# Kernel tuning notes

Measured on AMD Instinct MI355X. Metric: run time of the kernel, lower is better.

The kernel has to match this reference:

```python
import jax, jax.numpy as jnp
import numpy as np

N_NODES = 100000    # nodes in river network
N_PATHS = 1000000   # number of (src, dst) routing paths
MAX_DELAY = 16
DT = 1.0
CASCADE = 1.0
T = int(MAX_DELAY / DT)        # expanded time window (assert in original)
E = 8000000                    # total flattened path-node entries


def setup_inputs() -> dict:
    key = jax.random.key(0)
    k1, k2, k3 = jax.random.split(key, 3)
    params = jax.random.uniform(k1, (N_NODES,), dtype=jnp.float32)
    path_idxs = jnp.sort(jax.random.randint(k2, (E,), 0, N_PATHS, dtype=jnp.int32))
    path_nodes = jax.random.randint(k3, (E,), 0, N_NODES, dtype=jnp.int32)
    return {"params": params, "path_idxs": path_idxs, "path_nodes": path_nodes}


def reference(params, path_idxs, path_nodes):
    # irf_fn 'linear_storage': per-node linear-reservoir impulse response h(t)=exp(-t/k)/k
    k = params + 0.5                                  # storage const in [0.5, 1.5)
    t = jnp.arange(T, dtype=params.dtype) * DT        # [T]
    irfs = jnp.exp(-t[None, :] / k[:, None]) / k[:, None]   # [N, T]
    # frequency domain
    irfs_freq = jnp.fft.rfft(irfs, n=T, axis=-1)      # [N, F] complex
    # irf_agg 'log_triton': cascade-combine IRFs along each path = product of
    # transfer functions, done in log domain: gather logs, segment-sum per path.
    log_freq = jnp.log(irfs_freq)                     # [N, F] complex log
    gathered = log_freq[path_nodes]                   # [E, F] irregular gather
    agg_re = jax.ops.segment_sum(gathered.real, path_idxs, num_segments=N_PATHS)
    agg_im = jax.ops.segment_sum(gathered.imag, path_idxs, num_segments=N_PATHS)
    agg_log = (agg_re + 1j * agg_im) * CASCADE        # [P, F]
    irfs_freq_agg = jnp.exp(agg_log)
    # back to time domain
    irfs_agg = jnp.fft.irfft(irfs_freq_agg, n=T, axis=-1)   # [P, T]
    irfs_agg = jax.nn.relu(irfs_agg)
    irfs_agg = jnp.flip(irfs_agg, -1)                 # sampler.phi_k is identity for dt=1
    irfs_agg = irfs_agg / jnp.sum(irfs_agg, -1, keepdims=True)
    return irfs_agg                                   # COO values; coords scatter is a storage step
```

## Files before the change

### kernel.cpp

```cpp
#include <hip/hip_runtime.h>
#include <math.h>

#define N_NODES  100000
#define N_PATHS  1000000
#define E_TOT    8000000
#define NF       9
#define TAB_U32  25000
#define EB       1024
#define EPT      2
#define PB       256
#define RCH      4096

#define RMIN 0.135330f
#define RMAX 0.513420f
#define QSCALE (255.0f / (RMAX - RMIN))
#define DEQ    ((RMAX - RMIN) / 255.0f)

__device__ __constant__ float COS16[16] = {
  1.0f,  0.92387953f,  0.70710678f,  0.38268343f,  0.0f, -0.38268343f, -0.70710678f, -0.92387953f,
 -1.0f, -0.92387953f, -0.70710678f, -0.38268343f,  0.0f,  0.38268343f,  0.70710678f,  0.92387953f };
__device__ __constant__ float SIN16[16] = {
  0.0f,  0.38268343f,  0.70710678f,  0.92387953f,  1.0f,  0.92387953f,  0.70710678f,  0.38268343f,
  0.0f, -0.38268343f, -0.70710678f, -0.92387953f, -1.0f, -0.92387953f, -0.70710678f, -0.38268343f };

__global__ void node_rq_kernel(const float* __restrict__ params,
                               unsigned char* __restrict__ rtab_q) {
    int n = blockIdx.x * blockDim.x + threadIdx.x;
    if (n >= N_NODES) return;
    float k = params[n] + 0.5f;
    float r = expf(-1.0f / k);
    float q = (r - RMIN) * QSCALE;
    q = fminf(fmaxf(q + 0.5f, 0.0f), 255.0f);
    rtab_q[n] = (unsigned char)q;
}

__device__ __forceinline__ void put_bounds(int a, int b, int e, int* __restrict__ start) {
    for (int p = a + 1; p <= b; ++p) start[p] = e;
}

__global__ __launch_bounds__(EB) void epass_kernel(const int* __restrict__ pidx,
                                                   const int* __restrict__ pnode,
                                                   const unsigned int* __restrict__ rtab_q,
                                                   int* __restrict__ start,
                                                   unsigned char* __restrict__ r8_all) {
    __shared__ unsigned int tab[TAB_U32];
    const unsigned char* tabb = (const unsigned char*)tab;
    int tid = threadIdx.x;
    for (int i = tid; i < TAB_U32; i += EB) tab[i] = rtab_q[i];
    __syncthreads();

    int base_q = blockIdx.x * EB * EPT;
#pragma unroll
    for (int g = 0; g < EPT; g++) {
        int q = base_q + g * EB + tid;
        if (q >= E_TOT / 4) break;
        int e = q * 4;
        int4 v = ((const int4*)pidx)[q];
        int4 w = ((const int4*)pnode)[q];
        uchar4 r;
        r.x = tabb[w.x];
        r.y = tabb[w.y];
        r.z = tabb[w.z];
        r.w = tabb[w.w];
        ((uchar4*)r8_all)[q] = r;
        int prev = (e == 0) ? -1 : pidx[e - 1];
        put_bounds(prev, v.x, e,     start);
        put_bounds(v.x,  v.y, e + 1, start);
        put_bounds(v.y,  v.z, e + 2, start);
        put_bounds(v.z,  v.w, e + 3, start);
        if (e + 4 == E_TOT) {
            for (int p = v.w + 1; p <= N_PATHS; ++p) start[p] = E_TOT;
        }
    }
}

__global__ __launch_bounds__(PB) void path_kernel(const int* __restrict__ start,
                                                  const unsigned char* __restrict__ r8_all,
                                                  float* __restrict__ out) {
    __shared__ unsigned char rch[RCH + 4];
    int tid = threadIdx.x;
    int p0 = blockIdx.x * PB;
    int p  = p0 + tid;
    int pend = (p0 + PB < N_PATHS) ? p0 + PB : N_PATHS;

    int blk_s = start[p0];
    int blk_e = start[pend];
    int s0 = 0, s1 = 0;
    if (p < N_PATHS) { s0 = start[p]; s1 = start[p + 1]; }

    float d0 = 1.0f, d8 = 1.0f;
    float dr[7], di[7];
#pragma unroll
    for (int f = 0; f < 7; f++) { dr[f] = 1.0f; di[f] = 0.0f; }

    const unsigned int* r8w = (const unsigned int*)r8_all;
    for (int ab = blk_s & ~3; ab < blk_e; ab += RCH) {
        int wlen = (blk_e - ab < RCH) ? (blk_e - ab) : RCH;
        int nw = (wlen + 3) >> 2;
        __syncthreads();
        for (int j = tid; j < nw; j += PB)
            ((unsigned int*)rch)[j] = r8w[(ab >> 2) + j];
        __syncthreads();

        int lo = (s0 > ab) ? s0 : ab;
        int hi = (s1 < ab + wlen) ? s1 : ab + wlen;
        int n = hi - lo;
        int bi = lo - ab;
        for (int j = 0; j < n; j += 4) {
            float ra = fmaf((float)rch[bi + j], DEQ, RMIN);
            float rb = (j + 1 < n) ? fmaf((float)rch[bi + j + 1], DEQ, RMIN) : 0.0f;
            float rc = (j + 2 < n) ? fmaf((float)rch[bi + j + 2], DEQ, RMIN) : 0.0f;
            float rd = (j + 3 < n) ? fmaf((float)rch[bi + j + 3], DEQ, RMIN) : 0.0f;
            float sab = ra + rb, qab = ra * rb;
            float scd = rc + rd, qcd = rc * rd;
            float e1 = sab + scd;
            float e2 = fmaf(sab, scd, qab + qcd);
            float e3 = fmaf(qab, scd, qcd * sab);
            float e4 = qab * qcd;
#pragma unroll
            for (int f = 1; f <= 7; f++) {
                float tr = fmaf(-e1, COS16[f], 1.0f);
                tr = fmaf( e2, COS16[(2 * f) & 15], tr);
                tr = fmaf(-e3, COS16[(3 * f) & 15], tr);
                tr = fmaf( e4, COS16[(4 * f) & 15], tr);
                float ti = e1 * SIN16[f];
                ti = fmaf(-e2, SIN16[(2 * f) & 15], ti);
                ti = fmaf( e3, SIN16[(3 * f) & 15], ti);
                ti = fmaf(-e4, SIN16[(4 * f) & 15], ti);
                float a = dr[f - 1], b = di[f - 1];
                dr[f - 1] = fmaf(a, tr, -b * ti);
                di[f - 1] = fmaf(a, ti,  b * tr);
            }
            d0 *= ((1.0f - e1) + (e2 - e3)) + e4;
            d8 *= ((1.0f + e1) + (e2 + e3)) + e4;
        }
    }

    if (p >= N_PATHS) return;

    float Xr[NF], Xi[NF];
    Xr[0] = 1.0f; Xi[0] = 0.0f;
#pragma unroll
    for (int f = 1; f < 8; f++) {
        float a = dr[f - 1], b = di[f - 1];
        float m = fmaf(a, a, b * b);
        float inv = d0 * __builtin_amdgcn_rcpf(m);
        Xr[f] =  a * inv;
        Xi[f] = -b * inv;
    }
    Xr[8] = d0 * __builtin_amdgcn_rcpf(d8); Xi[8] = 0.0f;

    float xt[16];
    float ssum = 0.0f;
#pragma unroll
    for (int t = 0; t < 16; t++) {
        float acc = Xr[0] + ((t & 1) ? -Xr[8] : Xr[8]);
#pragma unroll
        for (int f = 1; f < 8; f++) {
            int kk = (f * t) & 15;
            acc = fmaf(2.0f * Xr[f], COS16[kk], acc);
            acc = fmaf(-2.0f * Xi[f], SIN16[kk], acc);
        }
        acc *= (1.0f / 16.0f);
        acc = fmaxf(acc, 0.0f);
        xt[t] = acc;
        ssum += acc;
    }

    float invs = __builtin_amdgcn_rcpf(ssum);
    float4* op4 = (float4*)(out + (size_t)p * 16);
    op4[0] = make_float4(xt[15] * invs, xt[14] * invs, xt[13] * invs, xt[12] * invs);
    op4[1] = make_float4(xt[11] * invs, xt[10] * invs, xt[9]  * invs, xt[8]  * invs);
    op4[2] = make_float4(xt[7]  * invs, xt[6]  * invs, xt[5]  * invs, xt[4]  * invs);
    op4[3] = make_float4(xt[3]  * invs, xt[2]  * invs, xt[1]  * invs, xt[0]  * invs);
}

extern "C" void kernel_launch(void* const* d_in, const int* in_sizes, int n_in,
                              void* d_out, int out_size, void* d_ws, size_t ws_size,
                              hipStream_t stream) {
    const float* params = (const float*)d_in[0];
    const int* path_idxs = (const int*)d_in[1];
    const int* path_nodes = (const int*)d_in[2];
    float* out = (float*)d_out;

    size_t off_rq    = 0;
    size_t off_start = (off_rq + (size_t)N_NODES + 1023) & ~(size_t)1023;
    size_t off_r8    = (off_start + (size_t)(N_PATHS + 1) * 4 + 1023) & ~(size_t)1023;

    unsigned char* rtab_q = (unsigned char*)d_ws + off_rq;
    int* start = (int*)((char*)d_ws + off_start);
    unsigned char* r8_all = (unsigned char*)d_ws + off_r8;

    {
        int threads = 256;
        int blocks = (N_NODES + threads - 1) / threads;
        node_rq_kernel<<<blocks, threads, 0, stream>>>(params, rtab_q);
    }
    {
        int per_block = EB * EPT;
        int blocks = (E_TOT / 4 + per_block - 1) / per_block;
        epass_kernel<<<blocks, EB, 0, stream>>>(path_idxs, path_nodes,
                                                (const unsigned int*)rtab_q,
                                                start, r8_all);
    }
    {
        int blocks = (N_PATHS + PB - 1) / PB;
        path_kernel<<<blocks, PB, 0, stream>>>(start, r8_all, out);
    }
}
```

Measured before the change: 143.3 us.

## Read path bytes directly from global memory and exploit inverse-DFT symmetry

```diff
diff --git a/kernel.cpp b/kernel.cpp
--- a/kernel.cpp
+++ b/kernel.cpp
@@ -7,9 +7,8 @@
 #define NF       9
 #define TAB_U32  25000
 #define EB       1024
-#define EPT      2
+#define EPT      4
 #define PB       256
-#define RCH      4096
 
 #define RMIN 0.135330f
 #define RMAX 0.513420f
@@ -75,70 +74,59 @@
 }
 
 __global__ __launch_bounds__(PB) void path_kernel(const int* __restrict__ start,
-                                                  const unsigned char* __restrict__ r8_all,
+                                                  const unsigned int* __restrict__ r8w,
                                                   float* __restrict__ out) {
-    __shared__ unsigned char rch[RCH + 4];
-    int tid = threadIdx.x;
-    int p0 = blockIdx.x * PB;
-    int p  = p0 + tid;
-    int pend = (p0 + PB < N_PATHS) ? p0 + PB : N_PATHS;
-
-    int blk_s = start[p0];
-    int blk_e = start[pend];
-    int s0 = 0, s1 = 0;
-    if (p < N_PATHS) { s0 = start[p]; s1 = start[p + 1]; }
+    int p = blockIdx.x * PB + threadIdx.x;
+    if (p >= N_PATHS) return;
+
+    int s0 = start[p];
+    int s1 = start[p + 1];
+    int len = s1 - s0;
+    int nq = (len + 3) >> 2;
+    int a0 = s0 >> 2;
+    unsigned sh = (unsigned)(s0 & 3) * 8u;
 
     float d0 = 1.0f, d8 = 1.0f;
     float dr[7], di[7];
 #pragma unroll
     for (int f = 0; f < 7; f++) { dr[f] = 1.0f; di[f] = 0.0f; }
 
-    const unsigned int* r8w = (const unsigned int*)r8_all;
-    for (int ab = blk_s & ~3; ab < blk_e; ab += RCH) {
-        int wlen = (blk_e - ab < RCH) ? (blk_e - ab) : RCH;
-        int nw = (wlen + 3) >> 2;
-        __syncthreads();
-        for (int j = tid; j < nw; j += PB)
-            ((unsigned int*)rch)[j] = r8w[(ab >> 2) + j];
-        __syncthreads();
-
-        int lo = (s0 > ab) ? s0 : ab;
-        int hi = (s1 < ab + wlen) ? s1 : ab + wlen;
-        int n = hi - lo;
-        int bi = lo - ab;
-        for (int j = 0; j < n; j += 4) {
-            float ra = fmaf((float)rch[bi + j], DEQ, RMIN);
-            float rb = (j + 1 < n) ? fmaf((float)rch[bi + j + 1], DEQ, RMIN) : 0.0f;
-            float rc = (j + 2 < n) ? fmaf((float)rch[bi + j + 2], DEQ, RMIN) : 0.0f;
-            float rd = (j + 3 < n) ? fmaf((float)rch[bi + j + 3], DEQ, RMIN) : 0.0f;
-            float sab = ra + rb, qab = ra * rb;
-            float scd = rc + rd, qcd = rc * rd;
-            float e1 = sab + scd;
-            float e2 = fmaf(sab, scd, qab + qcd);
-            float e3 = fmaf(qab, scd, qcd * sab);
-            float e4 = qab * qcd;
-#pragma unroll
-            for (int f = 1; f <= 7; f++) {
-                float tr = fmaf(-e1, COS16[f], 1.0f);
-                tr = fmaf( e2, COS16[(2 * f) & 15], tr);
-                tr = fmaf(-e3, COS16[(3 * f) & 15], tr);
-                tr = fmaf( e4, COS16[(4 * f) & 15], tr);
-                float ti = e1 * SIN16[f];
-                ti = fmaf(-e2, SIN16[(2 * f) & 15], ti);
-                ti = fmaf( e3, SIN16[(3 * f) & 15], ti);
-                ti = fmaf(-e4, SIN16[(4 * f) & 15], ti);
-                float a = dr[f - 1], b = di[f - 1];
-                dr[f - 1] = fmaf(a, tr, -b * ti);
-                di[f - 1] = fmaf(a, ti,  b * tr);
-            }
-            d0 *= ((1.0f - e1) + (e2 - e3)) + e4;
-            d8 *= ((1.0f + e1) + (e2 + e3)) + e4;
+    unsigned cur = (nq > 0) ? r8w[a0] : 0u;
+    for (int q = 0; q < nq; q++) {
+        int w = a0 + q + 1;
+        unsigned nxt = (w < E_TOT / 4) ? r8w[w] : 0u;
+        unsigned grp = (unsigned)(((((unsigned long long)nxt) << 32) | cur) >> sh);
+        cur = nxt;
+        int rem = len - 4 * q;
+        float ra = fmaf((float)(grp & 255u), DEQ, RMIN);
+        float rb = (rem > 1) ? fmaf((float)((grp >> 8) & 255u), DEQ, RMIN) : 0.0f;
+        float rc = (rem > 2) ? fmaf((float)((grp >> 16) & 255u), DEQ, RMIN) : 0.0f;
+        float rd = (rem > 3) ? fmaf((float)(grp >> 24), DEQ, RMIN) : 0.0f;
+        float sab = ra + rb, qab = ra * rb;
+        float scd = rc + rd, qcd = rc * rd;
+        float e1 = sab + scd;
+        float e2 = fmaf(sab, scd, qab + qcd);
+        float e3 = fmaf(qab, scd, qcd * sab);
+        float e4 = qab * qcd;
+#pragma unroll
+        for (int f = 1; f <= 7; f++) {
+            float tr = fmaf(-e1, COS16[f], 1.0f);
+            tr = fmaf( e2, COS16[(2 * f) & 15], tr);
+            tr = fmaf(-e3, COS16[(3 * f) & 15], tr);
+            tr = fmaf( e4, COS16[(4 * f) & 15], tr);
+            float ti = e1 * SIN16[f];
+            ti = fmaf(-e2, SIN16[(2 * f) & 15], ti);
+            ti = fmaf( e3, SIN16[(3 * f) & 15], ti);
+            ti = fmaf(-e4, SIN16[(4 * f) & 15], ti);
+            float a = dr[f - 1], b = di[f - 1];
+            dr[f - 1] = fmaf(a, tr, -b * ti);
+            di[f - 1] = fmaf(a, ti,  b * tr);
         }
-    }
-
-    if (p >= N_PATHS) return;
-
-    float Xr[NF], Xi[NF];
+        d0 *= ((1.0f - e1) + (e2 - e3)) + e4;
+        d8 *= ((1.0f + e1) + (e2 + e3)) + e4;
+    }
+
+    float Xr[8], Xi[8];
     Xr[0] = 1.0f; Xi[0] = 0.0f;
 #pragma unroll
     for (int f = 1; f < 8; f++) {
@@ -148,23 +136,33 @@
         Xr[f] =  a * inv;
         Xi[f] = -b * inv;
     }
-    Xr[8] = d0 * __builtin_amdgcn_rcpf(d8); Xi[8] = 0.0f;
+    float X8 = d0 * __builtin_amdgcn_rcpf(d8);
 
     float xt[16];
-    float ssum = 0.0f;
-#pragma unroll
-    for (int t = 0; t < 16; t++) {
-        float acc = Xr[0] + ((t & 1) ? -Xr[8] : Xr[8]);
+    float c0 = 0.0f, c8 = 0.0f;
+#pragma unroll
+    for (int f = 1; f < 8; f++) {
+        c0 += 2.0f * Xr[f];
+        c8 += (f & 1) ? -2.0f * Xr[f] : 2.0f * Xr[f];
+    }
+    xt[0] = fmaxf((Xr[0] + X8 + c0) * (1.0f / 16.0f), 0.0f);
+    xt[8] = fmaxf((Xr[0] + X8 + c8) * (1.0f / 16.0f), 0.0f);
+    float ssum = xt[0] + xt[8];
+#pragma unroll
+    for (int t = 1; t < 8; t++) {
+        float Ct = 0.0f, St = 0.0f;
 #pragma unroll
         for (int f = 1; f < 8; f++) {
             int kk = (f * t) & 15;
-            acc = fmaf(2.0f * Xr[f], COS16[kk], acc);
-            acc = fmaf(-2.0f * Xi[f], SIN16[kk], acc);
+            Ct = fmaf(2.0f * Xr[f], COS16[kk], Ct);
+            St = fmaf(2.0f * Xi[f], SIN16[kk], St);
         }
-        acc *= (1.0f / 16.0f);
-        acc = fmaxf(acc, 0.0f);
-        xt[t] = acc;
-        ssum += acc;
+        float base = Xr[0] + ((t & 1) ? -X8 : X8) + Ct;
+        float xa = fmaxf((base - St) * (1.0f / 16.0f), 0.0f);
+        float xb = fmaxf((base + St) * (1.0f / 16.0f), 0.0f);
+        xt[t] = xa;
+        xt[16 - t] = xb;
+        ssum += xa + xb;
     }
 
     float invs = __builtin_amdgcn_rcpf(ssum);
@@ -205,6 +203,6 @@
     }
     {
         int blocks = (N_PATHS + PB - 1) / PB;
-        path_kernel<<<blocks, PB, 0, stream>>>(start, r8_all, out);
-    }
-}
+        path_kernel<<<blocks, PB, 0, stream>>>(start, (const unsigned int*)r8_all, out);
+    }
+}
```

New measurement: 142.2 us. Within noise of the previous version (-0.7%).
